# Performance work log

Measured on AMD Instinct MI355X. Metric: run time of the kernel, lower is better.

## Reference

```python
import jax, jax.numpy as jnp
import numpy as np

NENTITY = 200000
NRELATION = 500
HIDDEN = 256
GAMMA = 12.0
EPS = 2.0
EMB_RANGE = (GAMMA + EPS) / HIDDEN


def setup_inputs() -> dict:
    key = jax.random.key(0)
    ks = jax.random.split(key, 8)
    B, NEG = 256, 1024
    head = jax.random.randint(ks[0], (B, 1), 0, NENTITY)
    tail = jax.random.randint(ks[1], (B, NEG), 0, NENTITY)
    relation = jax.random.randint(ks[2], (B,), 0, NRELATION)
    entity_emb = jax.random.uniform(ks[3], (NENTITY, HIDDEN), jnp.float32, -EMB_RANGE, EMB_RANGE)
    relation_emb = jax.random.uniform(ks[4], (NRELATION, 2 * HIDDEN), jnp.float32, -EMB_RANGE, EMB_RANGE)
    lim = 1.0 / np.sqrt(2 * HIDDEN)
    W_fc = jax.random.uniform(ks[5], (HIDDEN, 2 * HIDDEN), jnp.float32, -lim, lim)
    b_fc = jax.random.uniform(ks[6], (HIDDEN,), jnp.float32, -lim, lim)
    return {"head": head, "tail": tail, "relation": relation,
            "entity_emb": entity_emb, "relation_emb": relation_emb,
            "W_fc": W_fc, "b_fc": b_fc}


def _l2_normalize(x):
    # F.normalize(x, p=2, dim=-1): x / max(||x||_2, 1e-12)
    n = jnp.sqrt(jnp.sum(x * x, axis=-1, keepdims=True))
    return x / jnp.maximum(n, 1e-12)


def reference(head, tail, relation, entity_emb, relation_emb, W_fc, b_fc):
    # gather embeddings
    h = entity_emb[head]                      # [B, 1,   d]
    t = entity_emb[tail]                      # [B, NEG, d]
    r = relation_emb[relation][:, None, :]    # [B, 1, 2d]
    re_head, re_tail = jnp.split(r, 2, axis=-1)   # each [B, 1, d]
    # broadcast relation halves to match head/tail sample counts, then concat
    re_h = jnp.broadcast_to(re_head, h.shape)
    re_t = jnp.broadcast_to(re_tail, t.shape)
    h_cat = jnp.concatenate([h, re_h], axis=-1)   # [B, 1,   2d]
    t_cat = jnp.concatenate([t, re_t], axis=-1)   # [B, NEG, 2d]
    # shared small FC (torch Linear: x @ W^T + b)
    h_fc = jnp.einsum('bnk,dk->bnd', h_cat, W_fc) + b_fc
    t_fc = jnp.einsum('bnk,dk->bnd', t_cat, W_fc) + b_fc
    h_n = _l2_normalize(h_fc)
    t_n = _l2_normalize(t_fc)
    diff = h_n - t_n                              # [B, NEG, d]
    score = GAMMA - jnp.sum(jnp.abs(diff), axis=2)  # [B, NEG]
    return score
```

## Files before the change

### kernel.cpp

```cpp
#include <hip/hip_runtime.h>
#include <math.h>

#define HIDDEN 256
#define NEG 1024
#define NBATCH 256
#define GAMMA_F 12.0f
#define BM 64

typedef short v8s __attribute__((ext_vector_type(8)));
typedef float v4f __attribute__((ext_vector_type(4)));

__device__ __forceinline__ short f2bf(float x) {
    unsigned int u = __float_as_uint(x);
    u = (u + 0x7fffu + ((u >> 16) & 1u)) >> 16;
    return (short)u;
}

__global__ __launch_bounds__(256) void prep_kernel(
    const int* __restrict__ head, const int* __restrict__ relation,
    const float* __restrict__ entity_emb, const float* __restrict__ relation_emb,
    const float* __restrict__ W_fc, const float* __restrict__ b_fc,
    short* __restrict__ W1bf, float* __restrict__ h_n, float* __restrict__ rel_part)
{
    const int b = blockIdx.x;
    const int t = threadIdx.x;

    W1bf[b * HIDDEN + t] = f2bf(W_fc[(size_t)b * 2 * HIDDEN + t]);

    __shared__ float xh[2 * HIDDEN];
    __shared__ float xt[HIDDEN];
    __shared__ float red[256];

    const int hidx = head[b];
    const int r = relation[b];
    xh[t]          = entity_emb[(size_t)hidx * HIDDEN + t];
    xh[HIDDEN + t] = relation_emb[(size_t)r * 2 * HIDDEN + t];
    xt[t]          = relation_emb[(size_t)r * 2 * HIDDEN + HIDDEN + t];
    __syncthreads();

    const float4* wrow = reinterpret_cast<const float4*>(W_fc + (size_t)t * 2 * HIDDEN);
    float hf = b_fc[t];
    float rp = b_fc[t];
    #pragma unroll 4
    for (int kk = 0; kk < HIDDEN / 4; ++kk) {
        float4 w = wrow[kk];
        hf += xh[4*kk+0]*w.x + xh[4*kk+1]*w.y + xh[4*kk+2]*w.z + xh[4*kk+3]*w.w;
    }
    #pragma unroll 4
    for (int kk = 0; kk < HIDDEN / 4; ++kk) {
        float4 w = wrow[HIDDEN/4 + kk];
        hf += xh[HIDDEN+4*kk+0]*w.x + xh[HIDDEN+4*kk+1]*w.y + xh[HIDDEN+4*kk+2]*w.z + xh[HIDDEN+4*kk+3]*w.w;
        rp += xt[4*kk+0]*w.x + xt[4*kk+1]*w.y + xt[4*kk+2]*w.z + xt[4*kk+3]*w.w;
    }
    rel_part[b * HIDDEN + t] = rp;

    red[t] = hf * hf;
    __syncthreads();
    for (int s = 128; s > 0; s >>= 1) {
        if (t < s) red[t] += red[t + s];
        __syncthreads();
    }
    const float norm = sqrtf(red[0]);
    h_n[b * HIDDEN + t] = hf / fmaxf(norm, 1e-12f);
}

__global__ __launch_bounds__(256, 2) void score_kernel(
    const int* __restrict__ tail, const float* __restrict__ entity_emb,
    const short* __restrict__ W1bf, const float* __restrict__ h_n,
    const float* __restrict__ rel_part, float* __restrict__ out)
{
    __shared__ __align__(16) short As[BM * HIDDEN];
    __shared__ float ssq_lds[4][BM];
    __shared__ float l1_lds[4][BM];

    const int t  = threadIdx.x;
    const int m0 = blockIdx.x * BM;
    const int b  = blockIdx.x >> 4;

    const int c = t & 15;
    const int g = (t >> 4) & 3;
    const int w = t >> 6;
    const int l = t & 63;

    int rows[4];
    #pragma unroll
    for (int mt = 0; mt < 4; ++mt) rows[mt] = tail[m0 + mt * 16 + c];

    #pragma unroll
    for (int i = 0; i < 8; ++i) {
        const int s  = w + 4 * i;
        const int kt = s & 7;
        const int mt = s >> 3;
        const float4* src = reinterpret_cast<const float4*>(
            entity_emb + (size_t)rows[mt] * HIDDEN + (kt * 4 + g) * 8);
        float4 a0 = src[0], a1 = src[1];
        v8s v;
        v[0]=f2bf(a0.x); v[1]=f2bf(a0.y); v[2]=f2bf(a0.z); v[3]=f2bf(a0.w);
        v[4]=f2bf(a1.x); v[5]=f2bf(a1.y); v[6]=f2bf(a1.z); v[7]=f2bf(a1.w);
        *reinterpret_cast<v8s*>(As + (t + 256 * i) * 8) = v;
    }

    v8s Bf[4][8];
    #pragma unroll
    for (int ntl = 0; ntl < 4; ++ntl) {
        const short* bsrc = W1bf + (size_t)(64 * w + ntl * 16 + c) * HIDDEN + g * 8;
        #pragma unroll
        for (int kt = 0; kt < 8; ++kt)
            Bf[ntl][kt] = *reinterpret_cast<const v8s*>(bsrc + kt * 32);
    }

    v4f acc[4][4];
    #pragma unroll
    for (int mt = 0; mt < 4; ++mt)
        #pragma unroll
        for (int ntl = 0; ntl < 4; ++ntl)
            acc[mt][ntl] = v4f{0.f, 0.f, 0.f, 0.f};

    __syncthreads();

    #pragma unroll
    for (int kt = 0; kt < 8; ++kt) {
        v8s a[4];
        #pragma unroll
        for (int mt = 0; mt < 4; ++mt)
            a[mt] = *reinterpret_cast<const v8s*>(As + (mt * 512 + kt * 64 + l) * 8);
        #pragma unroll
        for (int mt = 0; mt < 4; ++mt) {
            #pragma unroll
            for (int ntl = 0; ntl < 4; ++ntl)
                acc[mt][ntl] = __builtin_amdgcn_mfma_f32_16x16x32_bf16(
                    a[mt], Bf[ntl][kt], acc[mt][ntl], 0, 0, 0);
        }
    }

    float rlv[4], hnv[4];
    #pragma unroll
    for (int ntl = 0; ntl < 4; ++ntl) {
        const int n = 64 * w + ntl * 16 + c;
        rlv[ntl] = rel_part[b * HIDDEN + n];
        hnv[ntl] = h_n[b * HIDDEN + n];
    }

    #pragma unroll
    for (int mt = 0; mt < 4; ++mt) {
        float ssq[4] = {0.f, 0.f, 0.f, 0.f};
        #pragma unroll
        for (int ntl = 0; ntl < 4; ++ntl) {
            #pragma unroll
            for (int r = 0; r < 4; ++r) {
                float tf = acc[mt][ntl][r] + rlv[ntl];
                acc[mt][ntl][r] = tf;
                ssq[r] += tf * tf;
            }
        }
        #pragma unroll
        for (int mask = 1; mask < 16; mask <<= 1) {
            #pragma unroll
            for (int r = 0; r < 4; ++r) ssq[r] += __shfl_xor(ssq[r], mask);
        }
        if (c == 0) {
            #pragma unroll
            for (int r = 0; r < 4; ++r) ssq_lds[w][mt * 16 + g * 4 + r] = ssq[r];
        }
    }
    __syncthreads();

    #pragma unroll
    for (int mt = 0; mt < 4; ++mt) {
        float rn[4], s1[4] = {0.f, 0.f, 0.f, 0.f};
        #pragma unroll
        for (int r = 0; r < 4; ++r) {
            const int m = mt * 16 + g * 4 + r;
            float tot = ssq_lds[0][m] + ssq_lds[1][m] + ssq_lds[2][m] + ssq_lds[3][m];
            rn[r] = 1.f / fmaxf(sqrtf(tot), 1e-12f);
        }
        #pragma unroll
        for (int ntl = 0; ntl < 4; ++ntl) {
            #pragma unroll
            for (int r = 0; r < 4; ++r)
                s1[r] += fabsf(hnv[ntl] - acc[mt][ntl][r] * rn[r]);
        }
        #pragma unroll
        for (int mask = 1; mask < 16; mask <<= 1) {
            #pragma unroll
            for (int r = 0; r < 4; ++r) s1[r] += __shfl_xor(s1[r], mask);
        }
        if (c == 0) {
            #pragma unroll
            for (int r = 0; r < 4; ++r) l1_lds[w][mt * 16 + g * 4 + r] = s1[r];
        }
    }
    __syncthreads();

    if (t < BM) {
        out[m0 + t] = GAMMA_F -
            (l1_lds[0][t] + l1_lds[1][t] + l1_lds[2][t] + l1_lds[3][t]);
    }
}

extern "C" void kernel_launch(void* const* d_in, const int* in_sizes, int n_in,
                              void* d_out, int out_size, void* d_ws, size_t ws_size,
                              hipStream_t stream)
{
    const int*   head         = (const int*)d_in[0];
    const int*   tail         = (const int*)d_in[1];
    const int*   relation     = (const int*)d_in[2];
    const float* entity_emb   = (const float*)d_in[3];
    const float* relation_emb = (const float*)d_in[4];
    const float* W_fc         = (const float*)d_in[5];
    const float* b_fc         = (const float*)d_in[6];
    float* out = (float*)d_out;

    short* W1bf     = (short*)d_ws;
    float* h_n      = (float*)((char*)d_ws + 131072);
    float* rel_part = (float*)((char*)d_ws + 131072 + 262144);

    prep_kernel<<<NBATCH, 256, 0, stream>>>(head, relation, entity_emb, relation_emb,
                                            W_fc, b_fc, W1bf, h_n, rel_part);
    score_kernel<<<(NBATCH * NEG) / BM, 256, 0, stream>>>(tail, entity_emb, W1bf,
                                                          h_n, rel_part, out);
}
```

Baseline: 367.1 us.

## Software-pipeline tail-row gathers across tiles with double-buffered LDS in persistent-ish blocks

The score kernel now gives each block 8 consecutive 32-row tiles of the same batch instead of one 64-row tile. It prefetches the next tile's gathered entity rows into registers while the current tile is converted and multiplied, using a double-buffered LDS A tile. W fragments are reloaded from global memory on every k-step instead of being held in registers, which frees registers so occupancy can rise to 4 blocks per CU. The aim is to hide the random-gather latency. The risks are extra W reload traffic and more barriers per tile.

```diff
diff --git a/kernel.cpp b/kernel.cpp
--- a/kernel.cpp
+++ b/kernel.cpp
@@ -5,7 +5,9 @@
 #define NEG 1024
 #define NBATCH 256
 #define GAMMA_F 12.0f
-#define BM 64
+#define BM 32
+#define NTILES 8
+#define NBLK 1024
 
 typedef short v8s __attribute__((ext_vector_type(8)));
 typedef float v4f __attribute__((ext_vector_type(4)));
@@ -64,74 +66,26 @@
     h_n[b * HIDDEN + t] = hf / fmaxf(norm, 1e-12f);
 }
 
-__global__ __launch_bounds__(256, 2) void score_kernel(
+__global__ __launch_bounds__(256, 4) void score_kernel(
     const int* __restrict__ tail, const float* __restrict__ entity_emb,
     const short* __restrict__ W1bf, const float* __restrict__ h_n,
     const float* __restrict__ rel_part, float* __restrict__ out)
 {
-    __shared__ __align__(16) short As[BM * HIDDEN];
+    __shared__ __align__(16) short As[2][BM * HIDDEN];
+    __shared__ int tails[NTILES * BM];
     __shared__ float ssq_lds[4][BM];
     __shared__ float l1_lds[4][BM];
 
-    const int t  = threadIdx.x;
-    const int m0 = blockIdx.x * BM;
-    const int b  = blockIdx.x >> 4;
-
-    const int c = t & 15;
-    const int g = (t >> 4) & 3;
-    const int w = t >> 6;
-    const int l = t & 63;
-
-    int rows[4];
-    #pragma unroll
-    for (int mt = 0; mt < 4; ++mt) rows[mt] = tail[m0 + mt * 16 + c];
-
-    #pragma unroll
-    for (int i = 0; i < 8; ++i) {
-        const int s  = w + 4 * i;
-        const int kt = s & 7;
-        const int mt = s >> 3;
-        const float4* src = reinterpret_cast<const float4*>(
-            entity_emb + (size_t)rows[mt] * HIDDEN + (kt * 4 + g) * 8);
-        float4 a0 = src[0], a1 = src[1];
-        v8s v;
-        v[0]=f2bf(a0.x); v[1]=f2bf(a0.y); v[2]=f2bf(a0.z); v[3]=f2bf(a0.w);
-        v[4]=f2bf(a1.x); v[5]=f2bf(a1.y); v[6]=f2bf(a1.z); v[7]=f2bf(a1.w);
-        *reinterpret_cast<v8s*>(As + (t + 256 * i) * 8) = v;
-    }
-
-    v8s Bf[4][8];
-    #pragma unroll
-    for (int ntl = 0; ntl < 4; ++ntl) {
-        const short* bsrc = W1bf + (size_t)(64 * w + ntl * 16 + c) * HIDDEN + g * 8;
-        #pragma unroll
-        for (int kt = 0; kt < 8; ++kt)
-            Bf[ntl][kt] = *reinterpret_cast<const v8s*>(bsrc + kt * 32);
-    }
-
-    v4f acc[4][4];
-    #pragma unroll
-    for (int mt = 0; mt < 4; ++mt)
-        #pragma unroll
-        for (int ntl = 0; ntl < 4; ++ntl)
-            acc[mt][ntl] = v4f{0.f, 0.f, 0.f, 0.f};
-
-    __syncthreads();
-
-    #pragma unroll
-    for (int kt = 0; kt < 8; ++kt) {
-        v8s a[4];
-        #pragma unroll
-        for (int mt = 0; mt < 4; ++mt)
-            a[mt] = *reinterpret_cast<const v8s*>(As + (mt * 512 + kt * 64 + l) * 8);
-        #pragma unroll
-        for (int mt = 0; mt < 4; ++mt) {
-            #pragma unroll
-            for (int ntl = 0; ntl < 4; ++ntl)
-                acc[mt][ntl] = __builtin_amdgcn_mfma_f32_16x16x32_bf16(
-                    a[mt], Bf[ntl][kt], acc[mt][ntl], 0, 0, 0);
-        }
-    }
+    const int t = threadIdx.x;
+    const int w   = t >> 6;
+    const int l   = t & 63;
+    const int c   = t & 15;
+    const int g   = (t >> 4) & 3;
+    const int kt0 = t >> 6;
+    const int base = blockIdx.x * NTILES;
+    const int b    = blockIdx.x >> 2;
+
+    tails[t] = tail[base * BM + t];
 
     float rlv[4], hnv[4];
     #pragma unroll
@@ -141,60 +95,119 @@
         hnv[ntl] = h_n[b * HIDDEN + n];
     }
 
+    __syncthreads();
+
+    auto issue = [&](int j, float4* ld) {
+        const int r0 = tails[j * BM + c];
+        const int r1 = tails[j * BM + 16 + c];
+        const float* p0 = entity_emb + (size_t)r0 * HIDDEN + kt0 * 32 + g * 8;
+        const float* p1 = entity_emb + (size_t)r1 * HIDDEN + kt0 * 32 + g * 8;
+        ld[0] = reinterpret_cast<const float4*>(p0)[0];
+        ld[1] = reinterpret_cast<const float4*>(p0)[1];
+        ld[2] = reinterpret_cast<const float4*>(p0 + 128)[0];
+        ld[3] = reinterpret_cast<const float4*>(p0 + 128)[1];
+        ld[4] = reinterpret_cast<const float4*>(p1)[0];
+        ld[5] = reinterpret_cast<const float4*>(p1)[1];
+        ld[6] = reinterpret_cast<const float4*>(p1 + 128)[0];
+        ld[7] = reinterpret_cast<const float4*>(p1 + 128)[1];
+    };
+
+    float4 ld[8];
+    issue(0, ld);
+
     #pragma unroll
-    for (int mt = 0; mt < 4; ++mt) {
-        float ssq[4] = {0.f, 0.f, 0.f, 0.f};
-        #pragma unroll
-        for (int ntl = 0; ntl < 4; ++ntl) {
+    for (int j = 0; j < NTILES; ++j) {
+        const int cur = j & 1;
+
+        short* dst = As[cur] + t * 8;
+        #pragma unroll
+        for (int i = 0; i < 4; ++i) {
+            float4 a0 = ld[2 * i], a1 = ld[2 * i + 1];
+            v8s v;
+            v[0]=f2bf(a0.x); v[1]=f2bf(a0.y); v[2]=f2bf(a0.z); v[3]=f2bf(a0.w);
+            v[4]=f2bf(a1.x); v[5]=f2bf(a1.y); v[6]=f2bf(a1.z); v[7]=f2bf(a1.w);
+            *reinterpret_cast<v8s*>(dst + i * 2048) = v;
+        }
+
+        if (j < NTILES - 1) issue(j + 1, ld);
+
+        __syncthreads();
+
+        v4f acc[2][4];
+        #pragma unroll
+        for (int mt = 0; mt < 2; ++mt)
+            #pragma unroll
+            for (int ntl = 0; ntl < 4; ++ntl)
+                acc[mt][ntl] = v4f{0.f, 0.f, 0.f, 0.f};
+
+        #pragma unroll
+        for (int kt = 0; kt < 8; ++kt) {
+            v8s a0 = *reinterpret_cast<const v8s*>(As[cur] + (kt * 64 + l) * 8);
+            v8s a1 = *reinterpret_cast<const v8s*>(As[cur] + (512 + kt * 64 + l) * 8);
+            #pragma unroll
+            for (int ntl = 0; ntl < 4; ++ntl) {
+                v8s bf = *reinterpret_cast<const v8s*>(
+                    W1bf + (size_t)(64 * w + ntl * 16 + c) * HIDDEN + kt * 32 + g * 8);
+                acc[0][ntl] = __builtin_amdgcn_mfma_f32_16x16x32_bf16(a0, bf, acc[0][ntl], 0, 0, 0);
+                acc[1][ntl] = __builtin_amdgcn_mfma_f32_16x16x32_bf16(a1, bf, acc[1][ntl], 0, 0, 0);
+            }
+        }
+
+        #pragma unroll
+        for (int mt = 0; mt < 2; ++mt) {
+            float ssq[4] = {0.f, 0.f, 0.f, 0.f};
+            #pragma unroll
+            for (int ntl = 0; ntl < 4; ++ntl) {
+                #pragma unroll
+                for (int r = 0; r < 4; ++r) {
+                    float tf = acc[mt][ntl][r] + rlv[ntl];
+                    acc[mt][ntl][r] = tf;
+                    ssq[r] += tf * tf;
+                }
+            }
+            #pragma unroll
+            for (int mask = 1; mask < 16; mask <<= 1) {
+                #pragma unroll
+                for (int r = 0; r < 4; ++r) ssq[r] += __shfl_xor(ssq[r], mask);
+            }
+            if (c == 0) {
+                #pragma unroll
+                for (int r = 0; r < 4; ++r) ssq_lds[w][mt * 16 + g * 4 + r] = ssq[r];
+            }
+        }
+        __syncthreads();
+
+        #pragma unroll
+        for (int mt = 0; mt < 2; ++mt) {
+            float rn[4], s1[4] = {0.f, 0.f, 0.f, 0.f};
             #pragma unroll
             for (int r = 0; r < 4; ++r) {
-                float tf = acc[mt][ntl][r] + rlv[ntl];
-                acc[mt][ntl][r] = tf;
-                ssq[r] += tf * tf;
-            }
-        }
-        #pragma unroll
-        for (int mask = 1; mask < 16; mask <<= 1) {
-            #pragma unroll
-            for (int r = 0; r < 4; ++r) ssq[r] += __shfl_xor(ssq[r], mask);
-        }
-        if (c == 0) {
-            #pragma unroll
-            for (int r = 0; r < 4; ++r) ssq_lds[w][mt * 16 + g * 4 + r] = ssq[r];
-        }
-    }
-    __syncthreads();
-
-    #pragma unroll
-    for (int mt = 0; mt < 4; ++mt) {
-        float rn[4], s1[4] = {0.f, 0.f, 0.f, 0.f};
-        #pragma unroll
-        for (int r = 0; r < 4; ++r) {
-            const int m = mt * 16 + g * 4 + r;
-            float tot = ssq_lds[0][m] + ssq_lds[1][m] + ssq_lds[2][m] + ssq_lds[3][m];
-            rn[r] = 1.f / fmaxf(sqrtf(tot), 1e-12f);
-        }
-        #pragma unroll
-        for (int ntl = 0; ntl < 4; ++ntl) {
-            #pragma unroll
-            for (int r = 0; r < 4; ++r)
-                s1[r] += fabsf(hnv[ntl] - acc[mt][ntl][r] * rn[r]);
-        }
-        #pragma unroll
-        for (int mask = 1; mask < 16; mask <<= 1) {
-            #pragma unroll
-            for (int r = 0; r < 4; ++r) s1[r] += __shfl_xor(s1[r], mask);
-        }
-        if (c == 0) {
-            #pragma unroll
-            for (int r = 0; r < 4; ++r) l1_lds[w][mt * 16 + g * 4 + r] = s1[r];
-        }
-    }
-    __syncthreads();
-
-    if (t < BM) {
-        out[m0 + t] = GAMMA_F -
-            (l1_lds[0][t] + l1_lds[1][t] + l1_lds[2][t] + l1_lds[3][t]);
+                const int m = mt * 16 + g * 4 + r;
+                float tot = ssq_lds[0][m] + ssq_lds[1][m] + ssq_lds[2][m] + ssq_lds[3][m];
+                rn[r] = 1.f / fmaxf(sqrtf(tot), 1e-12f);
+            }
+            #pragma unroll
+            for (int ntl = 0; ntl < 4; ++ntl) {
+                #pragma unroll
+                for (int r = 0; r < 4; ++r)
+                    s1[r] += fabsf(hnv[ntl] - acc[mt][ntl][r] * rn[r]);
+            }
+            #pragma unroll
+            for (int mask = 1; mask < 16; mask <<= 1) {
+                #pragma unroll
+                for (int r = 0; r < 4; ++r) s1[r] += __shfl_xor(s1[r], mask);
+            }
+            if (c == 0) {
+                #pragma unroll
+                for (int r = 0; r < 4; ++r) l1_lds[w][mt * 16 + g * 4 + r] = s1[r];
+            }
+        }
+        __syncthreads();
+
+        if (t < BM) {
+            out[(base + j) * BM + t] = GAMMA_F -
+                (l1_lds[0][t] + l1_lds[1][t] + l1_lds[2][t] + l1_lds[3][t]);
+        }
     }
 }
 
@@ -217,6 +230,6 @@
 
     prep_kernel<<<NBATCH, 256, 0, stream>>>(head, relation, entity_emb, relation_emb,
                                             W_fc, b_fc, W1bf, h_n, rel_part);
-    score_kernel<<<(NBATCH * NEG) / BM, 256, 0, stream>>>(tail, entity_emb, W1bf,
-                                                          h_n, rel_part, out);
-}
+    score_kernel<<<NBLK, 256, 0, stream>>>(tail, entity_emb, W1bf,
+                                           h_n, rel_part, out);
+}
```

Result: slower. 462.4 us (+25.9%).

## Persistent score kernel with double-buffered async global-to-LDS gathers

Applied to the files above, without the earlier changes.

Makes each score block persistent over 8 tiles of 32 tail rows. Tail embedding rows are streamed straight into a double-buffered, XOR-swizzled fp32 LDS buffer with global_load_lds, so the next tile's gather overlaps the current tile's MFMA and normalisation work. The bf16 weight fragments are loaded once per block instead of once per tile. The bf16 conversion moves to the LDS read side through a cheaper perm-based round-half-up pack, which changes rounding slightly compared with round-to-nearest-even. The fp32 LDS buffers double LDS use, and the loop adds hand-written waitcnt and barrier synchronisation.

```diff
diff --git a/kernel.cpp b/kernel.cpp
--- a/kernel.cpp
+++ b/kernel.cpp
@@ -5,15 +5,30 @@
 #define NEG 1024
 #define NBATCH 256
 #define GAMMA_F 12.0f
-#define BM 64
+#define BM 32
+#define NTILES 8
+#define NBLK 1024
 
 typedef short v8s __attribute__((ext_vector_type(8)));
 typedef float v4f __attribute__((ext_vector_type(4)));
+typedef unsigned int u32;
+
+#define LDS_BARRIER() asm volatile("s_waitcnt lgkmcnt(0)\n\ts_barrier" ::: "memory")
 
 __device__ __forceinline__ short f2bf(float x) {
-    unsigned int u = __float_as_uint(x);
+    u32 u = __float_as_uint(x);
     u = (u + 0x7fffu + ((u >> 16) & 1u)) >> 16;
     return (short)u;
+}
+
+__device__ __forceinline__ u32 rhu(float f) { return __float_as_uint(f) + 0x8000u; }
+__device__ __forceinline__ v8s pack8(const float4& x0, const float4& x1) {
+    int4 fr;
+    fr.x = __builtin_amdgcn_perm(rhu(x0.y), rhu(x0.x), 0x07060302u);
+    fr.y = __builtin_amdgcn_perm(rhu(x0.w), rhu(x0.z), 0x07060302u);
+    fr.z = __builtin_amdgcn_perm(rhu(x1.y), rhu(x1.x), 0x07060302u);
+    fr.w = __builtin_amdgcn_perm(rhu(x1.w), rhu(x1.z), 0x07060302u);
+    return __builtin_bit_cast(v8s, fr);
 }
 
 __global__ __launch_bounds__(256) void prep_kernel(
@@ -69,69 +84,19 @@
     const short* __restrict__ W1bf, const float* __restrict__ h_n,
     const float* __restrict__ rel_part, float* __restrict__ out)
 {
-    __shared__ __align__(16) short As[BM * HIDDEN];
+    __shared__ __align__(16) float Asf[2][BM * HIDDEN];
+    __shared__ int tails[NTILES * BM];
     __shared__ float ssq_lds[4][BM];
     __shared__ float l1_lds[4][BM];
 
-    const int t  = threadIdx.x;
-    const int m0 = blockIdx.x * BM;
-    const int b  = blockIdx.x >> 4;
-
+    const int t = threadIdx.x;
+    const int w = t >> 6;
+    const int l = t & 63;
     const int c = t & 15;
     const int g = (t >> 4) & 3;
-    const int w = t >> 6;
-    const int l = t & 63;
-
-    int rows[4];
-    #pragma unroll
-    for (int mt = 0; mt < 4; ++mt) rows[mt] = tail[m0 + mt * 16 + c];
-
-    #pragma unroll
-    for (int i = 0; i < 8; ++i) {
-        const int s  = w + 4 * i;
-        const int kt = s & 7;
-        const int mt = s >> 3;
-        const float4* src = reinterpret_cast<const float4*>(
-            entity_emb + (size_t)rows[mt] * HIDDEN + (kt * 4 + g) * 8);
-        float4 a0 = src[0], a1 = src[1];
-        v8s v;
-        v[0]=f2bf(a0.x); v[1]=f2bf(a0.y); v[2]=f2bf(a0.z); v[3]=f2bf(a0.w);
-        v[4]=f2bf(a1.x); v[5]=f2bf(a1.y); v[6]=f2bf(a1.z); v[7]=f2bf(a1.w);
-        *reinterpret_cast<v8s*>(As + (t + 256 * i) * 8) = v;
-    }
-
-    v8s Bf[4][8];
-    #pragma unroll
-    for (int ntl = 0; ntl < 4; ++ntl) {
-        const short* bsrc = W1bf + (size_t)(64 * w + ntl * 16 + c) * HIDDEN + g * 8;
-        #pragma unroll
-        for (int kt = 0; kt < 8; ++kt)
-            Bf[ntl][kt] = *reinterpret_cast<const v8s*>(bsrc + kt * 32);
-    }
-
-    v4f acc[4][4];
-    #pragma unroll
-    for (int mt = 0; mt < 4; ++mt)
-        #pragma unroll
-        for (int ntl = 0; ntl < 4; ++ntl)
-            acc[mt][ntl] = v4f{0.f, 0.f, 0.f, 0.f};
-
-    __syncthreads();
-
-    #pragma unroll
-    for (int kt = 0; kt < 8; ++kt) {
-        v8s a[4];
-        #pragma unroll
-        for (int mt = 0; mt < 4; ++mt)
-            a[mt] = *reinterpret_cast<const v8s*>(As + (mt * 512 + kt * 64 + l) * 8);
-        #pragma unroll
-        for (int mt = 0; mt < 4; ++mt) {
-            #pragma unroll
-            for (int ntl = 0; ntl < 4; ++ntl)
-                acc[mt][ntl] = __builtin_amdgcn_mfma_f32_16x16x32_bf16(
-                    a[mt], Bf[ntl][kt], acc[mt][ntl], 0, 0, 0);
-        }
-    }
+    const int b = blockIdx.x >> 2;
+
+    tails[t] = tail[blockIdx.x * (NTILES * BM) + t];
 
     float rlv[4], hnv[4];
     #pragma unroll
@@ -141,60 +106,126 @@
         hnv[ntl] = h_n[b * HIDDEN + n];
     }
 
+    v8s Bf[4][8];
     #pragma unroll
-    for (int mt = 0; mt < 4; ++mt) {
-        float ssq[4] = {0.f, 0.f, 0.f, 0.f};
-        #pragma unroll
-        for (int ntl = 0; ntl < 4; ++ntl) {
+    for (int ntl = 0; ntl < 4; ++ntl) {
+        const short* bsrc = W1bf + (size_t)(64 * w + ntl * 16 + c) * HIDDEN + g * 8;
+        #pragma unroll
+        for (int kt = 0; kt < 8; ++kt)
+            Bf[ntl][kt] = *reinterpret_cast<const v8s*>(bsrc + kt * 32);
+    }
+
+    __syncthreads();
+
+    auto issue = [&](int j, int buf) {
+        #pragma unroll
+        for (int i = 0; i < 8; ++i) {
+            const int r = w * 8 + i;
+            const int row = tails[j * BM + r];
+            const float* src = entity_emb + (size_t)row * HIDDEN + ((l ^ (r & 7)) << 2);
+            __builtin_amdgcn_global_load_lds(
+                (const __attribute__((address_space(1))) u32*)src,
+                (__attribute__((address_space(3))) u32*)&Asf[buf][r * HIDDEN],
+                16, 0, 0);
+        }
+    };
+
+    issue(0, 0);
+
+    #pragma unroll 1
+    for (int j = 0; j < NTILES; ++j) {
+        const int cur = j & 1;
+
+        if (j + 1 < NTILES) {
+            issue(j + 1, cur ^ 1);
+            asm volatile("s_waitcnt vmcnt(8)" ::: "memory");
+        } else {
+            asm volatile("s_waitcnt vmcnt(0)" ::: "memory");
+        }
+        asm volatile("s_barrier" ::: "memory");
+
+        v4f acc[2][4];
+        #pragma unroll
+        for (int mt = 0; mt < 2; ++mt)
+            #pragma unroll
+            for (int ntl = 0; ntl < 4; ++ntl)
+                acc[mt][ntl] = v4f{0.f, 0.f, 0.f, 0.f};
+
+        const float* a0base = &Asf[cur][c * HIDDEN];
+        const float* a1base = &Asf[cur][(16 + c) * HIDDEN];
+        const int swz = c & 7;
+
+        #pragma unroll
+        for (int kt = 0; kt < 8; ++kt) {
+            const int u0 = kt * 8 + g * 2;
+            float4 x0 = *reinterpret_cast<const float4*>(a0base + (((u0    ) ^ swz) << 2));
+            float4 x1 = *reinterpret_cast<const float4*>(a0base + (((u0 + 1) ^ swz) << 2));
+            float4 y0 = *reinterpret_cast<const float4*>(a1base + (((u0    ) ^ swz) << 2));
+            float4 y1 = *reinterpret_cast<const float4*>(a1base + (((u0 + 1) ^ swz) << 2));
+            v8s a0 = pack8(x0, x1);
+            v8s a1 = pack8(y0, y1);
+            #pragma unroll
+            for (int ntl = 0; ntl < 4; ++ntl) {
+                acc[0][ntl] = __builtin_amdgcn_mfma_f32_16x16x32_bf16(a0, Bf[ntl][kt], acc[0][ntl], 0, 0, 0);
+                acc[1][ntl] = __builtin_amdgcn_mfma_f32_16x16x32_bf16(a1, Bf[ntl][kt], acc[1][ntl], 0, 0, 0);
+            }
+        }
+
+        #pragma unroll
+        for (int mt = 0; mt < 2; ++mt) {
+            float ssq[4] = {0.f, 0.f, 0.f, 0.f};
+            #pragma unroll
+            for (int ntl = 0; ntl < 4; ++ntl) {
+                #pragma unroll
+                for (int r = 0; r < 4; ++r) {
+                    float tf = acc[mt][ntl][r] + rlv[ntl];
+                    acc[mt][ntl][r] = tf;
+                    ssq[r] += tf * tf;
+                }
+            }
+            #pragma unroll
+            for (int mask = 1; mask < 16; mask <<= 1) {
+                #pragma unroll
+                for (int r = 0; r < 4; ++r) ssq[r] += __shfl_xor(ssq[r], mask);
+            }
+            if (c == 0) {
+                #pragma unroll
+                for (int r = 0; r < 4; ++r) ssq_lds[w][mt * 16 + g * 4 + r] = ssq[r];
+            }
+        }
+        LDS_BARRIER();
+
+        #pragma unroll
+        for (int mt = 0; mt < 2; ++mt) {
+            float rn[4], s1[4] = {0.f, 0.f, 0.f, 0.f};
             #pragma unroll
             for (int r = 0; r < 4; ++r) {
-                float tf = acc[mt][ntl][r] + rlv[ntl];
-                acc[mt][ntl][r] = tf;
-                ssq[r] += tf * tf;
-            }
-        }
-        #pragma unroll
-        for (int mask = 1; mask < 16; mask <<= 1) {
-            #pragma unroll
-            for (int r = 0; r < 4; ++r) ssq[r] += __shfl_xor(ssq[r], mask);
-        }
-        if (c == 0) {
-            #pragma unroll
-            for (int r = 0; r < 4; ++r) ssq_lds[w][mt * 16 + g * 4 + r] = ssq[r];
-        }
-    }
-    __syncthreads();
-
-    #pragma unroll
-    for (int mt = 0; mt < 4; ++mt) {
-        float rn[4], s1[4] = {0.f, 0.f, 0.f, 0.f};
-        #pragma unroll
-        for (int r = 0; r < 4; ++r) {
-            const int m = mt * 16 + g * 4 + r;
-            float tot = ssq_lds[0][m] + ssq_lds[1][m] + ssq_lds[2][m] + ssq_lds[3][m];
-            rn[r] = 1.f / fmaxf(sqrtf(tot), 1e-12f);
-        }
-        #pragma unroll
-        for (int ntl = 0; ntl < 4; ++ntl) {
-            #pragma unroll
-            for (int r = 0; r < 4; ++r)
-                s1[r] += fabsf(hnv[ntl] - acc[mt][ntl][r] * rn[r]);
-        }
-        #pragma unroll
-        for (int mask = 1; mask < 16; mask <<= 1) {
-            #pragma unroll
-            for (int r = 0; r < 4; ++r) s1[r] += __shfl_xor(s1[r], mask);
-        }
-        if (c == 0) {
-            #pragma unroll
-            for (int r = 0; r < 4; ++r) l1_lds[w][mt * 16 + g * 4 + r] = s1[r];
-        }
-    }
-    __syncthreads();
-
-    if (t < BM) {
-        out[m0 + t] = GAMMA_F -
-            (l1_lds[0][t] + l1_lds[1][t] + l1_lds[2][t] + l1_lds[3][t]);
+                const int m = mt * 16 + g * 4 + r;
+                float tot = ssq_lds[0][m] + ssq_lds[1][m] + ssq_lds[2][m] + ssq_lds[3][m];
+                rn[r] = 1.f / fmaxf(sqrtf(tot), 1e-12f);
+            }
+            #pragma unroll
+            for (int ntl = 0; ntl < 4; ++ntl) {
+                #pragma unroll
+                for (int r = 0; r < 4; ++r)
+                    s1[r] += fabsf(hnv[ntl] - acc[mt][ntl][r] * rn[r]);
+            }
+            #pragma unroll
+            for (int mask = 1; mask < 16; mask <<= 1) {
+                #pragma unroll
+                for (int r = 0; r < 4; ++r) s1[r] += __shfl_xor(s1[r], mask);
+            }
+            if (c == 0) {
+                #pragma unroll
+                for (int r = 0; r < 4; ++r) l1_lds[w][mt * 16 + g * 4 + r] = s1[r];
+            }
+        }
+        LDS_BARRIER();
+
+        if (t < BM) {
+            out[blockIdx.x * (NTILES * BM) + j * BM + t] = GAMMA_F -
+                (l1_lds[0][t] + l1_lds[1][t] + l1_lds[2][t] + l1_lds[3][t]);
+        }
     }
 }
 
@@ -217,6 +248,6 @@
 
     prep_kernel<<<NBATCH, 256, 0, stream>>>(head, relation, entity_emb, relation_emb,
                                             W_fc, b_fc, W1bf, h_n, rel_part);
-    score_kernel<<<(NBATCH * NEG) / BM, 256, 0, stream>>>(tail, entity_emb, W1bf,
-                                                          h_n, rel_part, out);
-}
+    score_kernel<<<NBLK, 256, 0, stream>>>(tail, entity_emb, W1bf,
+                                           h_n, rel_part, out);
+}
```

Measured after the change: 349.0 us. 4.9% less time.
